# Kernel tuning notes

Measured on AMD Instinct MI355X. Metric: run time of the kernel, lower is better.

## Reference

```python
import jax, jax.numpy as jnp
import numpy as np

N, S, T, E, H = 4, 2048, 2048, 512, 8
HD = E // H  # head_dim = 64


def setup_inputs() -> dict:
    key0 = jax.random.key(0)
    ks = jax.random.split(key0, 12)
    sc = 1.0 / np.sqrt(E)
    inp = {
        "query": jax.random.normal(ks[0], (N, S, E), jnp.float32),
        "key": jax.random.normal(ks[1], (N, T, E), jnp.float32),
        "value": jax.random.normal(ks[2], (N, T, E), jnp.float32),
        "attn_mask": jnp.tril(jnp.ones((S, T), jnp.int32)),  # causal: 0 => masked
        # nn.Linear weights (out, in) and biases, torch convention y = x @ W.T + b
        "Wq": jax.random.normal(ks[3], (E, E), jnp.float32) * sc,
        "bq": jax.random.normal(ks[4], (E,), jnp.float32) * sc,
        "Wk": jax.random.normal(ks[5], (E, E), jnp.float32) * sc,
        "bk": jax.random.normal(ks[6], (E,), jnp.float32) * sc,
        "Wv": jax.random.normal(ks[7], (E, E), jnp.float32) * sc,
        "bv": jax.random.normal(ks[8], (E,), jnp.float32) * sc,
        "Wp": jax.random.normal(ks[9], (E, E), jnp.float32) * sc,
        "bp": jax.random.normal(ks[10], (E,), jnp.float32) * sc,
    }
    return inp


def reference(query, key, value, attn_mask, Wq, bq, Wk, bk, Wv, bv, Wp, bp):
    # QKV projections, split heads: (N, H, L, HD)
    q = (query @ Wq.T + bq).reshape(N, S, H, HD).transpose(0, 2, 1, 3)
    k = (key @ Wk.T + bk).reshape(N, T, H, HD).transpose(0, 2, 1, 3)
    v = (value @ Wv.T + bv).reshape(N, T, H, HD).transpose(0, 2, 1, 3)
    # scaled scores (N, H, S, T) -- intentionally materialized like the original
    e = jnp.einsum("nhsd,nhtd->nhst", q, k) / jnp.sqrt(jnp.float32(HD))
    e = jnp.where(attn_mask == 0, -jnp.inf, e)
    a = jax.nn.softmax(e, axis=-1)
    # dropout is identity in eval mode (reference runs deterministic/eval)
    y = jnp.einsum("nhst,nhtd->nhsd", a, v)
    y = y.transpose(0, 2, 1, 3).reshape(N, S, E)
    return y @ Wp.T + bp
```

## Files before the change

kernel.cpp:

```cpp
#include <hip/hip_runtime.h>


#define DEV __device__ __forceinline__

typedef unsigned short u16;
typedef unsigned int u32;
typedef __bf16 bf16x8 __attribute__((ext_vector_type(8)));
typedef float f32x4 __attribute__((ext_vector_type(4)));

#define MFMA_BF16(A, B, C) __builtin_amdgcn_mfma_f32_16x16x32_bf16(A, B, C, 0, 0, 0)

DEV u16 f2bf(float f) {
  u32 u = __builtin_bit_cast(u32, f);
  u += 0x7fffu + ((u >> 16) & 1u);
  return (u16)(u >> 16);
}

DEV void cp16(void* l, const void* g) {
  __builtin_amdgcn_global_load_lds(
      (const __attribute__((address_space(1))) u32*)g,
      (__attribute__((address_space(3))) u32*)l, 16, 0, 0);
}

#define WAIT_VM(N) asm volatile("s_waitcnt vmcnt(" #N ")" ::: "memory")
#define WAIT_VMLG  asm volatile("s_waitcnt vmcnt(0) lgkmcnt(0)" ::: "memory")
#define WAIT_LG    asm volatile("s_waitcnt lgkmcnt(0)" ::: "memory")
#define BARRIER    asm volatile("s_barrier" ::: "memory")

__global__ __launch_bounds__(256) void cast_all(
    const float* __restrict__ q, const float* __restrict__ k, const float* __restrict__ v,
    const float* __restrict__ wq, const float* __restrict__ wk,
    const float* __restrict__ wv, const float* __restrict__ wp,
    u16* qo, u16* ko, u16* vo, u16* wqo, u16* wko, u16* wvo, u16* wpo) {
  int b = blockIdx.x;
  const float* s;
  u16* d;
  int i;
  if (b < 12288) {
    int t = b >> 12;
    s = (t == 0) ? q : (t == 1) ? k : v;
    d = (t == 0) ? qo : (t == 1) ? ko : vo;
    i = (b & 4095) * 256 + threadIdx.x;
  } else {
    int t = (b - 12288) >> 8;
    s = (t == 0) ? wq : (t == 1) ? wk : (t == 2) ? wv : wp;
    d = (t == 0) ? wqo : (t == 1) ? wko : (t == 2) ? wvo : wpo;
    i = ((b - 12288) & 255) * 256 + threadIdx.x;
  }
  float4 f = ((const float4*)s)[i];
  ushort4 o;
  o.x = f2bf(f.x); o.y = f2bf(f.y); o.z = f2bf(f.z); o.w = f2bf(f.w);
  ((ushort4*)d)[i] = o;
}

DEV void gemm_stage(const u16* __restrict__ A, const u16* __restrict__ W,
                    u16* As, u16* Bs, int m0, int n0, int kt, int tid) {
#pragma unroll
  for (int i = 0; i < 2; ++i) {
    int c = tid + 256 * i;
    int row = c >> 2, kc = (c & 3) * 8;
    cp16(&As[c * 8], A + (m0 + row) * 512 + kt + kc);
    cp16(&Bs[c * 8], W + (n0 + row) * 512 + kt + kc);
  }
}

DEV void gemm_loop(const u16* __restrict__ A, const u16* __restrict__ W,
                   u16* As, u16* Bs,
                   int m0, int n0, int tid, f32x4 acc[4][4]) {
  const int lane = tid & 63, wid = tid >> 6;
  const int wm = wid & 1, wn = wid >> 1;
  const int l15 = lane & 15, l4 = lane >> 4;
  gemm_stage(A, W, As, Bs, m0, n0, 0, tid);
  gemm_stage(A, W, As + 4096, Bs + 4096, m0, n0, 32, tid);
  WAIT_VM(4);
  BARRIER;
  for (int it = 0; it < 16; ++it) {
    const u16* Ac = As + (it & 1) * 4096;
    const u16* Bc = Bs + (it & 1) * 4096;
    bf16x8 af[4], bfr[4];
#pragma unroll
    for (int f = 0; f < 4; ++f) {
      af[f]  = *(const bf16x8*)&Ac[(wm * 64 + f * 16 + l15) * 32 + l4 * 8];
      bfr[f] = *(const bf16x8*)&Bc[(wn * 64 + f * 16 + l15) * 32 + l4 * 8];
    }
    __builtin_amdgcn_s_setprio(1);
#pragma unroll
    for (int fm = 0; fm < 4; ++fm)
#pragma unroll
      for (int fn = 0; fn < 4; ++fn)
        acc[fm][fn] = MFMA_BF16(af[fm], bfr[fn], acc[fm][fn]);
    __builtin_amdgcn_s_setprio(0);
    if (it < 15) {
      WAIT_VMLG;
      BARRIER;
      if (it + 2 < 16)
        gemm_stage(A, W, As + (it & 1) * 4096, Bs + (it & 1) * 4096,
                   m0, n0, (it + 2) * 32, tid);
    }
  }
}

__global__ __launch_bounds__(256) void gemm_qkv(
    const u16* __restrict__ qx, const u16* __restrict__ kx, const u16* __restrict__ vx,
    const u16* __restrict__ wq, const u16* __restrict__ wk, const u16* __restrict__ wv,
    const float* __restrict__ bq, const float* __restrict__ bk, const float* __restrict__ bv,
    u16* qp, u16* kp, u16* vtO) {
  __shared__ u16 SH[17408];
  u16* As = SH;
  u16* Bs = SH + 8192;
  const int wsel = blockIdx.x >> 2;
  const u16* A = (wsel == 0) ? qx : (wsel == 1) ? kx : vx;
  const u16* W = (wsel == 0) ? wq : (wsel == 1) ? wk : wv;
  const float* bias = (wsel == 0) ? bq : (wsel == 1) ? bk : bv;
  const int n0 = (blockIdx.x & 3) * 128, m0 = blockIdx.y * 128;
  const int tid = threadIdx.x, lane = tid & 63, wid = tid >> 6;
  const int wm = wid & 1, wn = wid >> 1;
  const int l15 = lane & 15, l4 = lane >> 4;

  f32x4 acc[4][4] = {};
  gemm_loop(A, W, As, Bs, m0, n0, tid, acc);

  if (wsel == 2) {
    WAIT_LG;
    BARRIER;
    u16* Cs = SH;
#pragma unroll
    for (int fn = 0; fn < 4; ++fn) {
      int dl = wn * 64 + fn * 16 + l15;
      float bvv = bias[n0 + dl];
#pragma unroll
      for (int fm = 0; fm < 4; ++fm) {
        int trow = wm * 64 + fm * 16 + l4 * 4;
        int t64 = trow & 63;
        int pbase = (trow >> 6) * 64 + ((((t64 >> 5) << 2) | ((t64 >> 2) & 3)) << 3)
                    + (((t64 >> 4) & 1) << 2);
        ushort4 o;
        o.x = f2bf(acc[fm][fn][0] + bvv);
        o.y = f2bf(acc[fm][fn][1] + bvv);
        o.z = f2bf(acc[fm][fn][2] + bvv);
        o.w = f2bf(acc[fm][fn][3] + bvv);
        *(ushort4*)&Cs[dl * 136 + pbase] = o;
      }
    }
    WAIT_LG;
    BARRIER;
    const int nb = m0 >> 11, m0loc = m0 & 2047;
#pragma unroll
    for (int i = 0; i < 8; ++i) {
      int f = i * 256 + tid;
      int rowd = f >> 4, ch = (f & 15) * 8;
      uint4 x = *(const uint4*)&Cs[rowd * 136 + ch];
      *(uint4*)(vtO + (nb * 512 + n0 + rowd) * 2048 + m0loc + ch) = x;
    }
  } else {
    u16* C = (wsel == 0) ? qp : kp;
    const float osc = (wsel == 0) ? 0.18033688f : 1.0f;
#pragma unroll
    for (int fn = 0; fn < 4; ++fn) {
      int col = n0 + wn * 64 + fn * 16 + l15;
      float bvv = bias[col];
#pragma unroll
      for (int fm = 0; fm < 4; ++fm) {
        int rowb = m0 + wm * 64 + fm * 16 + l4 * 4;
#pragma unroll
        for (int r = 0; r < 4; ++r)
          C[(rowb + r) * 512 + col] = f2bf((acc[fm][fn][r] + bvv) * osc);
      }
    }
  }
}

__global__ __launch_bounds__(256) void gemm_out(const u16* __restrict__ A,
                                                const u16* __restrict__ W,
                                                const float* __restrict__ bias,
                                                float* __restrict__ C) {
  __shared__ u16 As[2 * 64 * 32];
  __shared__ u16 Bs[2 * 128 * 32];
  const int n0 = blockIdx.x * 128, m0 = blockIdx.y * 64;
  const int tid = threadIdx.x, lane = tid & 63, wid = tid >> 6;
  const int wm = wid & 1, wn = wid >> 1;
  const int l15 = lane & 15, l4 = lane >> 4;

  auto stage = [&](u16* Asb, u16* Bsb, int kt) {
    {
      int row = tid >> 2, kc = (tid & 3) * 8;
      cp16(&Asb[tid * 8], A + (m0 + row) * 512 + kt + kc);
    }
#pragma unroll
    for (int i = 0; i < 2; ++i) {
      int c = tid + 256 * i;
      int row = c >> 2, kc = (c & 3) * 8;
      cp16(&Bsb[c * 8], W + (n0 + row) * 512 + kt + kc);
    }
  };

  f32x4 acc[2][4] = {};
  stage(As, Bs, 0);
  stage(As + 2048, Bs + 4096, 32);
  WAIT_VM(3);
  BARRIER;
  for (int it = 0; it < 16; ++it) {
    const u16* Ac = As + (it & 1) * 2048;
    const u16* Bc = Bs + (it & 1) * 4096;
    bf16x8 af[2], bfr[4];
#pragma unroll
    for (int f = 0; f < 2; ++f)
      af[f] = *(const bf16x8*)&Ac[(wm * 32 + f * 16 + l15) * 32 + l4 * 8];
#pragma unroll
    for (int f = 0; f < 4; ++f)
      bfr[f] = *(const bf16x8*)&Bc[(wn * 64 + f * 16 + l15) * 32 + l4 * 8];
    __builtin_amdgcn_s_setprio(1);
#pragma unroll
    for (int fm = 0; fm < 2; ++fm)
#pragma unroll
      for (int fn = 0; fn < 4; ++fn)
        acc[fm][fn] = MFMA_BF16(af[fm], bfr[fn], acc[fm][fn]);
    __builtin_amdgcn_s_setprio(0);
    if (it < 15) {
      WAIT_VMLG;
      BARRIER;
      if (it + 2 < 16)
        stage(As + (it & 1) * 2048, Bs + (it & 1) * 4096, (it + 2) * 32);
    }
  }

#pragma unroll
  for (int fn = 0; fn < 4; ++fn) {
    int col = n0 + wn * 64 + fn * 16 + l15;
    float bvv = bias[col];
#pragma unroll
    for (int fm = 0; fm < 2; ++fm) {
      int rowb = m0 + wm * 32 + fm * 16 + l4 * 4;
#pragma unroll
      for (int r = 0; r < 4; ++r)
        C[(rowb + r) * 512 + col] = acc[fm][fn][r] + bvv;
    }
  }
}

__global__ __launch_bounds__(256) void attn_kernel(const u16* __restrict__ Qg,
                                                   const u16* __restrict__ Kg,
                                                   const u16* __restrict__ Vt,
                                                   u16* __restrict__ Yg,
                                                   float* __restrict__ Opart,
                                                   float* __restrict__ Lpart) {
  __shared__ u16 Ks[128 * 64];
  __shared__ u16 Vts[64 * 128];

  const int bid = blockIdx.x;
  int qt, nh, it0 = 0, half = 0;
  bool split;
  if (bid < 512) {
    qt = 16 + (bid >> 5); nh = bid & 31; split = true;
  } else if (bid < 576) {
    int i = bid - 512; qt = 14 + (i >> 5); nh = i & 31; split = false;
  } else if (bid < 640) {
    int i = bid - 576; qt = 30 + (i >> 5); nh = i & 31; it0 = 8; half = 1; split = true;
  } else {
    int g = bid - 640, c = 7 - (g >> 7), k = g & 127;
    if (k < 64) { qt = 2 * c - 2 + (k >> 5); nh = k & 31; split = false; }
    else { int k2 = k - 64; qt = 2 * c + 14 + (k2 >> 5); nh = k2 & 31; it0 = 8; half = 1; split = true; }
  }
  const int nt = (qt >> 1) + 1;
  const int itEnd = (split && half == 0) ? 8 : nt;

  const int n = nh >> 3, h = nh & 7;
  const int tid = threadIdx.x, lane = tid & 63, w = tid >> 6;
  const int l15 = lane & 15, l4 = lane >> 4;
  const int s0 = qt * 64;

  const u16* Kb = Kg + n * 2048 * 512 + h * 64;
  const u16* Vb = Vt + nh * 64 * 2048;

  const int qr = w * 16 + l15;
  const u16* qptr = Qg + (n * 2048 + s0 + qr) * 512 + h * 64;
  bf16x8 qf0 = __builtin_bit_cast(bf16x8, *(const uint4*)(qptr + l4 * 8));
  bf16x8 qf1 = __builtin_bit_cast(bf16x8, *(const uint4*)(qptr + 32 + l4 * 8));

  const u16* kSrc[4];
  const u16* vSrc[4];
  int kDst[4], vDst[4];
#pragma unroll
  for (int i = 0; i < 4; ++i) {
    int c = tid + 256 * i;
    int t = c >> 3, dg = (c & 7) ^ (t & 7);
    kSrc[i] = Kb + (it0 * 128 + t) * 512 + dg * 8;
    kDst[i] = c * 8;
    int d = c >> 4, x = c & 15;
    vSrc[i] = Vb + d * 2048 + it0 * 128 + ((x ^ (d & 15)) * 8);
    vDst[i] = c * 8;
  }

#pragma unroll
  for (int i = 0; i < 4; ++i) { cp16(&Ks[kDst[i]], kSrc[i]); kSrc[i] += 128 * 512; }
#pragma unroll
  for (int i = 0; i < 4; ++i) { cp16(&Vts[vDst[i]], vSrc[i]); vSrc[i] += 128; }

  WAIT_VM(4);
  BARRIER;

  f32x4 accO[4] = {};
  f32x4 lacc = {};
  const int sgl = s0 + w * 16 + l15;

  for (int it = it0; it < itEnd; ++it) {
    const int t0 = it * 128;
    const bool more = (it + 1 < itEnd);

    f32x4 st[8];
    __builtin_amdgcn_s_setprio(1);
#pragma unroll
    for (int fn = 0; fn < 8; ++fn) {
      int tr = fn * 16 + l15;
      bf16x8 k0 = *(const bf16x8*)&Ks[tr * 64 + ((l4 ^ (tr & 7)) * 8)];
      bf16x8 k1 = *(const bf16x8*)&Ks[tr * 64 + (((4 + l4) ^ (tr & 7)) * 8)];
      f32x4 a = {};
      a = MFMA_BF16(k0, qf0, a);
      st[fn] = MFMA_BF16(k1, qf1, a);
    }
    __builtin_amdgcn_s_setprio(0);

    WAIT_VMLG;
    BARRIER;
    if (more) {
#pragma unroll
      for (int i = 0; i < 4; ++i) { cp16(&Ks[kDst[i]], kSrc[i]); kSrc[i] += 128 * 512; }
    }

    const bool diag = (t0 + 128 > s0);
    if (diag) {
#pragma unroll
      for (int fn = 0; fn < 8; ++fn)
#pragma unroll
        for (int r = 0; r < 4; ++r) {
          int tg = t0 + fn * 16 + l4 * 4 + r;
          if (tg > sgl) st[fn][r] = -1e30f;
        }
    }
#pragma unroll
    for (int fn = 0; fn < 8; ++fn)
#pragma unroll
      for (int r = 0; r < 4; ++r)
        st[fn][r] = __builtin_amdgcn_exp2f(st[fn][r]);
    {
      f32x4 s4 = st[0] + st[1];
      s4 += st[2] + st[3];
      s4 += st[4] + st[5];
      s4 += st[6] + st[7];
      lacc += s4;
    }

    bf16x8 pa[4];
#pragma unroll
    for (int ks = 0; ks < 4; ++ks) {
      bf16x8 t;
      t[0] = (__bf16)st[2 * ks][0];     t[1] = (__bf16)st[2 * ks][1];
      t[2] = (__bf16)st[2 * ks][2];     t[3] = (__bf16)st[2 * ks][3];
      t[4] = (__bf16)st[2 * ks + 1][0]; t[5] = (__bf16)st[2 * ks + 1][1];
      t[6] = (__bf16)st[2 * ks + 1][2]; t[7] = (__bf16)st[2 * ks + 1][3];
      pa[ks] = t;
    }

    __builtin_amdgcn_s_setprio(1);
#pragma unroll
    for (int ks = 0; ks < 4; ++ks) {
#pragma unroll
      for (int fd = 0; fd < 4; ++fd) {
        int d = fd * 16 + l15;
        bf16x8 bv = *(const bf16x8*)&Vts[d * 128 + (((ks * 4 + l4) ^ l15) * 8)];
        accO[fd] = MFMA_BF16(pa[ks], bv, accO[fd]);
      }
    }
    __builtin_amdgcn_s_setprio(0);

    if (more) {
      WAIT_VMLG;
      BARRIER;
#pragma unroll
      for (int i = 0; i < 4; ++i) { cp16(&Vts[vDst[i]], vSrc[i]); vSrc[i] += 128; }
    }
  }

  float lr = lacc[0] + lacc[1] + lacc[2] + lacc[3];
  lr += __shfl_xor(lr, 16);
  lr += __shfl_xor(lr, 32);

  if (!split) {
    float lO[4];
#pragma unroll
    for (int r = 0; r < 4; ++r) lO[r] = __shfl(lr, (lane & 48) | (l4 * 4 + r));
#pragma unroll
    for (int fd = 0; fd < 4; ++fd)
#pragma unroll
      for (int r = 0; r < 4; ++r) {
        int row = s0 + w * 16 + l4 * 4 + r;
        int col = h * 64 + fd * 16 + l15;
        Yg[(n * 2048 + row) * 512 + col] = f2bf(accO[fd][r] / lO[r]);
      }
  } else {
    const int p = (qt - 16) * 32 + nh;
    float* Ob = Opart + (p * 2 + half) * 4096;
#pragma unroll
    for (int fd = 0; fd < 4; ++fd)
#pragma unroll
      for (int r = 0; r < 4; ++r)
        Ob[(fd * 4 + r) * 256 + tid] = accO[fd][r];
    if (l4 == 0) Lpart[(p * 2 + half) * 64 + w * 16 + l15] = lr;
  }
}

__global__ __launch_bounds__(256) void merge_o(const float* __restrict__ Opart,
                                               const float* __restrict__ Lpart,
                                               u16* __restrict__ Yg) {
  const int p = blockIdx.x;
  const int qt = 16 + (p >> 5), nh = p & 31;
  const int n = nh >> 3, h = nh & 7, s0 = qt * 64;
  const int tid = threadIdx.x, lane = tid & 63, w = tid >> 6;
  const int l15 = lane & 15, l4 = lane >> 4;
  const float* O1 = Opart + p * 8192;
  const float* O2 = O1 + 4096;
  const float* L1 = Lpart + p * 128;
  const float* L2 = L1 + 64;
  float lO[4];
#pragma unroll
  for (int r = 0; r < 4; ++r) {
    int row = w * 16 + l4 * 4 + r;
    lO[r] = L1[row] + L2[row];
  }
#pragma unroll
  for (int fd = 0; fd < 4; ++fd)
#pragma unroll
    for (int r = 0; r < 4; ++r) {
      float o = O1[(fd * 4 + r) * 256 + tid] + O2[(fd * 4 + r) * 256 + tid];
      int row = s0 + w * 16 + l4 * 4 + r;
      int col = h * 64 + fd * 16 + l15;
      Yg[(n * 2048 + row) * 512 + col] = f2bf(o / lO[r]);
    }
}

extern "C" void kernel_launch(void* const* d_in, const int* in_sizes, int n_in,
                              void* d_out, int out_size, void* d_ws, size_t ws_size,
                              hipStream_t stream) {
  (void)in_sizes; (void)n_in; (void)out_size; (void)ws_size;
  const float* query = (const float*)d_in[0];
  const float* key_  = (const float*)d_in[1];
  const float* value = (const float*)d_in[2];
  const float* Wq = (const float*)d_in[4];
  const float* bq = (const float*)d_in[5];
  const float* Wk = (const float*)d_in[6];
  const float* bk = (const float*)d_in[7];
  const float* Wv = (const float*)d_in[8];
  const float* bv = (const float*)d_in[9];
  const float* Wp = (const float*)d_in[10];
  const float* bp = (const float*)d_in[11];

  char* ws = (char*)d_ws;
  u16* qx  = (u16*)(ws);
  u16* kx  = (u16*)(ws + 8388608);
  u16* vx  = (u16*)(ws + 16777216);
  u16* wqx = (u16*)(ws + 25165824);
  u16* wkx = (u16*)(ws + 25690112);
  u16* wvx = (u16*)(ws + 26214400);
  u16* wpx = (u16*)(ws + 26738688);
  u16* qp  = (u16*)(ws + 27262976);
  u16* kp  = (u16*)(ws + 35651584);
  u16* vt  = (u16*)(ws + 44040192);
  u16* y   = qx;
  float* Opart = (float*)kx;
  float* Lpart = (float*)wqx;

  cast_all<<<13312, 256, 0, stream>>>(query, key_, value, Wq, Wk, Wv, Wp,
                                      qx, kx, vx, wqx, wkx, wvx, wpx);
  gemm_qkv<<<dim3(12, 64), 256, 0, stream>>>(qx, kx, vx, wqx, wkx, wvx,
                                             bq, bk, bv, qp, kp, vt);
  attn_kernel<<<1536, 256, 0, stream>>>(qp, kp, vt, y, Opart, Lpart);
  merge_o<<<512, 256, 0, stream>>>(Opart, Lpart, y);
  gemm_out<<<dim3(4, 128), 256, 0, stream>>>(y, wpx, bp, (float*)d_out);
}
```

Baseline: 191.2 us.

## Fuse fp32-to-bf16 activation cast into QKV projection GEMM loads

Removes the separate cast pass over query/key/value and instead has the QKV GEMM load fp32 activations directly into registers, convert to bf16, and write them to shared memory. A register-prefetch pipeline runs two k-steps ahead while the weights keep using async global-to-LDS copies. This avoids writing and re-reading a bf16 copy of the three large inputs. In exchange, each QKV block now reads twice as many bytes of A per tile and the GEMM main loop does extra conversion and register work. Rounding now uses the compiler's __bf16 conversion instead of the manual routine.

```diff
diff --git a/kernel.cpp b/kernel.cpp
--- a/kernel.cpp
+++ b/kernel.cpp
@@ -27,81 +27,29 @@
 #define WAIT_LG    asm volatile("s_waitcnt lgkmcnt(0)" ::: "memory")
 #define BARRIER    asm volatile("s_barrier" ::: "memory")
 
-__global__ __launch_bounds__(256) void cast_all(
-    const float* __restrict__ q, const float* __restrict__ k, const float* __restrict__ v,
-    const float* __restrict__ wq, const float* __restrict__ wk,
-    const float* __restrict__ wv, const float* __restrict__ wp,
-    u16* qo, u16* ko, u16* vo, u16* wqo, u16* wko, u16* wvo, u16* wpo) {
-  int b = blockIdx.x;
-  const float* s;
-  u16* d;
-  int i;
-  if (b < 12288) {
-    int t = b >> 12;
-    s = (t == 0) ? q : (t == 1) ? k : v;
-    d = (t == 0) ? qo : (t == 1) ? ko : vo;
-    i = (b & 4095) * 256 + threadIdx.x;
-  } else {
-    int t = (b - 12288) >> 8;
-    s = (t == 0) ? wq : (t == 1) ? wk : (t == 2) ? wv : wp;
-    d = (t == 0) ? wqo : (t == 1) ? wko : (t == 2) ? wvo : wpo;
-    i = ((b - 12288) & 255) * 256 + threadIdx.x;
-  }
+DEV bf16x8 cvt8(float4 a, float4 b) {
+  bf16x8 v;
+  v[0] = (__bf16)a.x; v[1] = (__bf16)a.y; v[2] = (__bf16)a.z; v[3] = (__bf16)a.w;
+  v[4] = (__bf16)b.x; v[5] = (__bf16)b.y; v[6] = (__bf16)b.z; v[7] = (__bf16)b.w;
+  return v;
+}
+
+__global__ __launch_bounds__(256) void cast_w(
+    const float* __restrict__ a, const float* __restrict__ b,
+    const float* __restrict__ c, const float* __restrict__ d2,
+    u16* ao, u16* bo, u16* co, u16* do_) {
+  int t = blockIdx.x >> 8;
+  const float* s = (t == 0) ? a : (t == 1) ? b : (t == 2) ? c : d2;
+  u16* d = (t == 0) ? ao : (t == 1) ? bo : (t == 2) ? co : do_;
+  int i = (blockIdx.x & 255) * 256 + threadIdx.x;
   float4 f = ((const float4*)s)[i];
   ushort4 o;
   o.x = f2bf(f.x); o.y = f2bf(f.y); o.z = f2bf(f.z); o.w = f2bf(f.w);
   ((ushort4*)d)[i] = o;
 }
 
-DEV void gemm_stage(const u16* __restrict__ A, const u16* __restrict__ W,
-                    u16* As, u16* Bs, int m0, int n0, int kt, int tid) {
-#pragma unroll
-  for (int i = 0; i < 2; ++i) {
-    int c = tid + 256 * i;
-    int row = c >> 2, kc = (c & 3) * 8;
-    cp16(&As[c * 8], A + (m0 + row) * 512 + kt + kc);
-    cp16(&Bs[c * 8], W + (n0 + row) * 512 + kt + kc);
-  }
-}
-
-DEV void gemm_loop(const u16* __restrict__ A, const u16* __restrict__ W,
-                   u16* As, u16* Bs,
-                   int m0, int n0, int tid, f32x4 acc[4][4]) {
-  const int lane = tid & 63, wid = tid >> 6;
-  const int wm = wid & 1, wn = wid >> 1;
-  const int l15 = lane & 15, l4 = lane >> 4;
-  gemm_stage(A, W, As, Bs, m0, n0, 0, tid);
-  gemm_stage(A, W, As + 4096, Bs + 4096, m0, n0, 32, tid);
-  WAIT_VM(4);
-  BARRIER;
-  for (int it = 0; it < 16; ++it) {
-    const u16* Ac = As + (it & 1) * 4096;
-    const u16* Bc = Bs + (it & 1) * 4096;
-    bf16x8 af[4], bfr[4];
-#pragma unroll
-    for (int f = 0; f < 4; ++f) {
-      af[f]  = *(const bf16x8*)&Ac[(wm * 64 + f * 16 + l15) * 32 + l4 * 8];
-      bfr[f] = *(const bf16x8*)&Bc[(wn * 64 + f * 16 + l15) * 32 + l4 * 8];
-    }
-    __builtin_amdgcn_s_setprio(1);
-#pragma unroll
-    for (int fm = 0; fm < 4; ++fm)
-#pragma unroll
-      for (int fn = 0; fn < 4; ++fn)
-        acc[fm][fn] = MFMA_BF16(af[fm], bfr[fn], acc[fm][fn]);
-    __builtin_amdgcn_s_setprio(0);
-    if (it < 15) {
-      WAIT_VMLG;
-      BARRIER;
-      if (it + 2 < 16)
-        gemm_stage(A, W, As + (it & 1) * 4096, Bs + (it & 1) * 4096,
-                   m0, n0, (it + 2) * 32, tid);
-    }
-  }
-}
-
 __global__ __launch_bounds__(256) void gemm_qkv(
-    const u16* __restrict__ qx, const u16* __restrict__ kx, const u16* __restrict__ vx,
+    const float* __restrict__ qf, const float* __restrict__ kf, const float* __restrict__ vf,
     const u16* __restrict__ wq, const u16* __restrict__ wk, const u16* __restrict__ wv,
     const float* __restrict__ bq, const float* __restrict__ bk, const float* __restrict__ bv,
     u16* qp, u16* kp, u16* vtO) {
@@ -109,7 +57,7 @@
   u16* As = SH;
   u16* Bs = SH + 8192;
   const int wsel = blockIdx.x >> 2;
-  const u16* A = (wsel == 0) ? qx : (wsel == 1) ? kx : vx;
+  const float* A = (wsel == 0) ? qf : (wsel == 1) ? kf : vf;
   const u16* W = (wsel == 0) ? wq : (wsel == 1) ? wk : wv;
   const float* bias = (wsel == 0) ? bq : (wsel == 1) ? bk : bv;
   const int n0 = (blockIdx.x & 3) * 128, m0 = blockIdx.y * 128;
@@ -117,8 +65,74 @@
   const int wm = wid & 1, wn = wid >> 1;
   const int l15 = lane & 15, l4 = lane >> 4;
 
+  const int r0 = tid >> 2, kc = (tid & 3) * 8;
+  const float* A0 = A + (m0 + r0) * 512 + kc;
+  const float* A1 = A + (m0 + r0 + 64) * 512 + kc;
+
+  auto stageB = [&](u16* Bsb, int kt) {
+#pragma unroll
+    for (int i = 0; i < 2; ++i) {
+      int c = tid + 256 * i;
+      int row = c >> 2, kcb = (c & 3) * 8;
+      cp16(&Bsb[c * 8], W + (n0 + row) * 512 + kt + kcb);
+    }
+  };
+
   f32x4 acc[4][4] = {};
-  gemm_loop(A, W, As, Bs, m0, n0, tid, acc);
+  {
+    float4 t00 = *(const float4*)(A0);
+    float4 t01 = *(const float4*)(A0 + 4);
+    float4 t02 = *(const float4*)(A1);
+    float4 t03 = *(const float4*)(A1 + 4);
+    float4 ca0 = *(const float4*)(A0 + 32);
+    float4 ca1 = *(const float4*)(A0 + 36);
+    float4 cb0 = *(const float4*)(A1 + 32);
+    float4 cb1 = *(const float4*)(A1 + 36);
+    stageB(Bs, 0);
+    stageB(Bs + 4096, 32);
+    *(bf16x8*)&As[tid * 8] = cvt8(t00, t01);
+    *(bf16x8*)&As[(tid + 256) * 8] = cvt8(t02, t03);
+    WAIT_VMLG;
+    BARRIER;
+
+    for (int it = 0; it < 16; ++it) {
+      if (it < 15) {
+        u16* Ad = As + ((it + 1) & 1) * 4096;
+        *(bf16x8*)&Ad[tid * 8] = cvt8(ca0, ca1);
+        *(bf16x8*)&Ad[(tid + 256) * 8] = cvt8(cb0, cb1);
+      }
+      float4 na0, na1, nb0, nb1;
+      if (it + 2 < 16) {
+        const float* P0 = A0 + (it + 2) * 32;
+        const float* P1 = A1 + (it + 2) * 32;
+        na0 = *(const float4*)(P0);
+        na1 = *(const float4*)(P0 + 4);
+        nb0 = *(const float4*)(P1);
+        nb1 = *(const float4*)(P1 + 4);
+      }
+      const u16* Ac = As + (it & 1) * 4096;
+      const u16* Bc = Bs + (it & 1) * 4096;
+      bf16x8 af[4], bfr[4];
+#pragma unroll
+      for (int f = 0; f < 4; ++f) {
+        af[f]  = *(const bf16x8*)&Ac[(wm * 64 + f * 16 + l15) * 32 + l4 * 8];
+        bfr[f] = *(const bf16x8*)&Bc[(wn * 64 + f * 16 + l15) * 32 + l4 * 8];
+      }
+      __builtin_amdgcn_s_setprio(1);
+#pragma unroll
+      for (int fm = 0; fm < 4; ++fm)
+#pragma unroll
+        for (int fn = 0; fn < 4; ++fn)
+          acc[fm][fn] = MFMA_BF16(af[fm], bfr[fn], acc[fm][fn]);
+      __builtin_amdgcn_s_setprio(0);
+      if (it < 15) {
+        WAIT_VMLG;
+        BARRIER;
+        if (it + 2 < 16) stageB(Bs + (it & 1) * 4096, (it + 2) * 32);
+        ca0 = na0; ca1 = na1; cb0 = nb0; cb1 = nb1;
+      }
+    }
+  }
 
   if (wsel == 2) {
     WAIT_LG;
@@ -455,7 +469,7 @@
   const float* bp = (const float*)d_in[11];
 
   char* ws = (char*)d_ws;
-  u16* qx  = (u16*)(ws);
+  u16* y   = (u16*)(ws);
   u16* kx  = (u16*)(ws + 8388608);
   u16* vx  = (u16*)(ws + 16777216);
   u16* wqx = (u16*)(ws + 25165824);
@@ -465,13 +479,11 @@
   u16* qp  = (u16*)(ws + 27262976);
   u16* kp  = (u16*)(ws + 35651584);
   u16* vt  = (u16*)(ws + 44040192);
-  u16* y   = qx;
   float* Opart = (float*)kx;
   float* Lpart = (float*)wqx;
 
-  cast_all<<<13312, 256, 0, stream>>>(query, key_, value, Wq, Wk, Wv, Wp,
-                                      qx, kx, vx, wqx, wkx, wvx, wpx);
-  gemm_qkv<<<dim3(12, 64), 256, 0, stream>>>(qx, kx, vx, wqx, wkx, wvx,
+  cast_w<<<1024, 256, 0, stream>>>(Wq, Wk, Wv, Wp, wqx, wkx, wvx, wpx);
+  gemm_qkv<<<dim3(12, 64), 256, 0, stream>>>(query, key_, value, wqx, wkx, wvx,
                                              bq, bk, bv, qp, kp, vt);
   attn_kernel<<<1536, 256, 0, stream>>>(qp, kp, vt, y, Opart, Lpart);
   merge_o<<<512, 256, 0, stream>>>(Opart, Lpart, y);
```

Result: no change. 192.9 us (+0.9%).
